# Optimization experiments

Measured on AMD Instinct MI355X. Metric: run time of the kernel, lower is better.

## Reference

```python
import jax, jax.numpy as jnp
import numpy as np

N, E, R, L = 20000, 160000, 3, 2
IN, HID, H, OUT = 64, 128, 16, 1
FH = HID // H   # per-head dim = 8
HD2 = HID // 2  # MLP bottleneck = 64


def setup_inputs() -> dict:
    key = jax.random.key(0)
    ks = iter(jax.random.split(key, 40))
    def w(*shape):
        return jax.random.normal(next(ks), shape, jnp.float32) * 0.05
    inp = dict(
        inputs=jax.random.normal(next(ks), (N, IN), jnp.float32),
        src=jax.random.randint(next(ks), (R, E), 0, N, dtype=jnp.int32),
        dst=jax.random.randint(next(ks), (R, E), 0, N, dtype=jnp.int32),
        e1_W=w(IN, HID), e1_b=jnp.zeros(HID), e_g=jnp.ones(HID), e_bt=jnp.zeros(HID),
        e2_W=w(HID, HID), e2_b=jnp.zeros(HID),
        gat_W=w(L, R, HID, HID), gat_al=w(L, R, H, FH), gat_ar=w(L, R, H, FH),
        gat_b=jnp.zeros((L, R, HID)),
        attn_p=w(L, R, HID),
        m1_W=w(L, HID, HD2), m1_b=jnp.zeros((L, HD2)), m_g=jnp.ones((L, HD2)), m_bt=jnp.zeros((L, HD2)),
        m2_W=w(L, HD2, HID), m2_b=jnp.zeros((L, HID)),
        d1_W=w(HID, HD2), d1_b=jnp.zeros(HD2), d_g=jnp.ones(HD2), d_bt=jnp.zeros(HD2),
        d2_W=w(HD2, OUT), d2_b=jnp.zeros(OUT),
    )
    return inp


def _bn(x, g, b):
    # BatchNorm1d, training mode: biased batch statistics, eps=1e-5
    mu = x.mean(0)
    var = jnp.mean((x - mu) ** 2, 0)
    return g * (x - mu) * jax.lax.rsqrt(var + 1e-5) + b


def _mlp(x, W1, b1, g, bt, W2, b2, skip=False):
    h = jax.nn.relu(_bn(x @ W1 + b1, g, bt))
    o = h @ W2 + b2
    return o + h if skip else o


def _gat(x, W, al, ar, b, src, dst):
    # single-relation DGL GATConv (feat_drop=attn_drop=0, neg_slope=0.2, bias)
    z = (x @ W).reshape(N, H, FH)                 # [N,H,FH]
    el = (z * al).sum(-1)                          # [N,H]
    er = (z * ar).sum(-1)                          # [N,H]
    e = jax.nn.leaky_relu(el[src] + er[dst], 0.2)  # [E,H]
    m = jax.ops.segment_max(e, dst, num_segments=N)
    m = jnp.where(jnp.isfinite(m), m, 0.0)
    ex = jnp.exp(e - m[dst])
    s = jax.ops.segment_sum(ex, dst, num_segments=N)
    alpha = ex / s[dst]                            # edge softmax over in-edges
    out = jax.ops.segment_sum(alpha[:, :, None] * z[src], dst, num_segments=N)
    return out.reshape(N, HID) + b                 # flatten heads + bias


def reference(inputs, src, dst, e1_W, e1_b, e_g, e_bt, e2_W, e2_b,
              gat_W, gat_al, gat_ar, gat_b, attn_p,
              m1_W, m1_b, m_g, m_bt, m2_W, m2_b,
              d1_W, d1_b, d_g, d_bt, d2_W, d2_b):
    h = _mlp(inputs, e1_W, e1_b, e_g, e_bt, e2_W, e2_b, skip=True)  # embed, skip
    gat_v = jax.vmap(_gat, in_axes=(None, 0, 0, 0, 0, 0, 0))        # over relations
    for l in range(L):
        stacked = gat_v(h, gat_W[l], gat_al[l], gat_ar[l], gat_b[l], src, dst)  # [R,N,HID]
        w = jax.nn.softmax(attn_p[l], axis=0)        # per-dim softmax over relations [R,HID]
        v = jnp.einsum('rnf,rf->nf', stacked, w)     # attn-weighted relation agg
        h = _mlp(v, m1_W[l], m1_b[l], m_g[l], m_bt[l], m2_W[l], m2_b[l]) + h
    return _mlp(h, d1_W, d1_b, d_g, d_bt, d2_W, d2_b)
```

## Files before the change

### kernel.cpp

```cpp
#include <hip/hip_runtime.h>
#include <math.h>

constexpr int kN   = 20000;
constexpr int kE   = 160000;
constexpr int kR   = 3;
constexpr int kL   = 2;
constexpr int kIN  = 64;
constexpr int kHID = 128;
constexpr int kH   = 16;
constexpr int kFH  = 8;
constexpr int kHD2 = 64;

typedef __bf16 bf16x8 __attribute__((ext_vector_type(8)));
typedef float  f32x4  __attribute__((ext_vector_type(4)));

__device__ __forceinline__ bf16x8 ldfrag(const __bf16* p) {
  return __builtin_bit_cast(bf16x8, *(const uint4*)p);
}
__device__ __forceinline__ f32x4 MF(bf16x8 a, bf16x8 b, f32x4 c) {
  return __builtin_amdgcn_mfma_f32_16x16x32_bf16(a, b, c, 0, 0, 0);
}

__device__ __forceinline__ void splitrow(const float* __restrict__ rowbase, int koff,
                                         bool bn, const float* scS, const float* shS,
                                         bf16x8& hi, bf16x8& lo) {
  float4 xa = *(const float4*)(rowbase + koff);
  float4 xb = *(const float4*)(rowbase + koff + 4);
  float x[8] = {xa.x, xa.y, xa.z, xa.w, xb.x, xb.y, xb.z, xb.w};
  union { __bf16 b[8]; bf16x8 v; } uh, ul;
#pragma unroll
  for (int e = 0; e < 8; e++) {
    float y = x[e];
    if (bn) y = fmaxf(fmaf(y, scS[koff + e], shS[koff + e]), 0.f);
    __bf16 hb = (__bf16)y;
    uh.b[e] = hb;
    ul.b[e] = (__bf16)(y - (float)hb);
  }
  hi = uh.v; lo = ul.v;
}

__global__ __launch_bounds__(256) void mgemm_kernel(
    const float* __restrict__ A, const __bf16* __restrict__ WT,
    const float* __restrict__ bias, const float* __restrict__ resf, int resmode,
    const float* __restrict__ bnstat, const float* __restrict__ bng,
    const float* __restrict__ bnbt, float invn,
    float* __restrict__ statS,
    float* __restrict__ Cf, __bf16* __restrict__ Chi,
    const float* __restrict__ alb, const float* __restrict__ arb,
    float* __restrict__ elb, float* __restrict__ erb,
    int n, int k, int m, long wstride, long cstride) {
  __shared__ __bf16 Bh[64][136];
  __shared__ __bf16 Bl[64][136];
  __shared__ float scS[128], shS[128];
  const int t  = threadIdx.x;
  const int w  = t >> 6;
  const int l  = t & 63;
  const int lr = l & 15;
  const int lg = l >> 4;
  const int rb = blockIdx.x * 128 + w * 32;
  const int c0 = blockIdx.y * 64;
  const __bf16* Whi = WT + (size_t)blockIdx.z * wstride;
  const __bf16* Wlo = Whi + (size_t)k * m;
  if (Chi) Chi += (size_t)blockIdx.z * cstride;
  const float* al = alb ? alb + blockIdx.z * kHID : nullptr;
  const float* ar = arb ? arb + blockIdx.z * kHID : nullptr;
  if (elb) { elb += blockIdx.z * 16; erb += blockIdx.z * 16; }

  const bool bn = bnstat != nullptr;
  if (bn && t < k) {
    float mu  = bnstat[t] * invn;
    float var = bnstat[k + t] * invn - mu * mu;
    float s = bng[t] * rsqrtf(var + 1e-5f);
    scS[t] = s; shS[t] = bnbt[t] - mu * s;
  }
  const int kseg = k >> 3;
  for (int idx = t; idx < 64 * kseg; idx += 256) {
    int col = idx / kseg, seg = idx - col * kseg;
    *(uint4*)&Bh[col][seg * 8] = *(const uint4*)&Whi[(size_t)(c0 + col) * k + seg * 8];
    *(uint4*)&Bl[col][seg * 8] = *(const uint4*)&Wlo[(size_t)(c0 + col) * k + seg * 8];
  }
  __syncthreads();

  int r0 = rb + lr;      if (r0 > n - 1) r0 = n - 1;
  int r1 = rb + 16 + lr; if (r1 > n - 1) r1 = n - 1;
  f32x4 acc[2][4] = {};

  for (int ks = 0; ks < (k >> 5); ks++) {
    const int koff = ks * 32 + lg * 8;
    bf16x8 a0h, a0l, a1h, a1l;
    splitrow(&A[(size_t)r0 * k], koff, bn, scS, shS, a0h, a0l);
    splitrow(&A[(size_t)r1 * k], koff, bn, scS, shS, a1h, a1l);
#pragma unroll
    for (int j = 0; j < 4; j++) {
      bf16x8 bh = ldfrag(&Bh[j * 16 + lr][koff]);
      bf16x8 bl = ldfrag(&Bl[j * 16 + lr][koff]);
      acc[0][j] = MF(a0h, bh, acc[0][j]);
      acc[0][j] = MF(a0l, bh, acc[0][j]);
      acc[0][j] = MF(a0h, bl, acc[0][j]);
      acc[1][j] = MF(a1h, bh, acc[1][j]);
      acc[1][j] = MF(a1l, bh, acc[1][j]);
      acc[1][j] = MF(a1h, bl, acc[1][j]);
    }
  }

  float s[4] = {}, s2[4] = {};
#pragma unroll
  for (int i = 0; i < 2; i++) {
#pragma unroll
    for (int q = 0; q < 4; q++) {
      int row = rb + i * 16 + lg * 4 + q;
      bool ok = row < n;
#pragma unroll
      for (int j = 0; j < 4; j++) {
        int col = c0 + j * 16 + lr;
        float v = acc[i][j][q];
        if (bias) v += bias[col];
        size_t off = (size_t)row * m + col;
        if (ok) {
          if (resmode == 1) v += resf[off];
          else if (resmode == 2) v += fmaxf(fmaf(resf[off], scS[col], shS[col]), 0.f);
          if (Cf) Cf[off] = v;
          if (Chi) Chi[off] = (__bf16)v;
          s[j] += v; s2[j] += v * v;
        }
      }
    }
  }
  if (statS) {
    __syncthreads();
    float* red = (float*)&Bh[0][0];
#pragma unroll
    for (int j = 0; j < 4; j++) {
      float a = s[j], b = s2[j];
      a += __shfl_xor(a, 16, 64); a += __shfl_xor(a, 32, 64);
      b += __shfl_xor(b, 16, 64); b += __shfl_xor(b, 32, 64);
      if (lg == 0) { red[w * 64 + j * 16 + lr] = a; red[256 + w * 64 + j * 16 + lr] = b; }
    }
    __syncthreads();
    if (t < 64) {
      float a = red[t] + red[64 + t] + red[128 + t] + red[192 + t];
      float b = red[256 + t] + red[320 + t] + red[384 + t] + red[448 + t];
      atomicAdd(&statS[c0 + t], a);
      atomicAdd(&statS[m + c0 + t], b);
    }
  }
  if (al) {
#pragma unroll
    for (int i = 0; i < 2; i++) {
#pragma unroll
      for (int q = 0; q < 4; q++) {
        int row = rb + i * 16 + lg * 4 + q;
#pragma unroll
        for (int j = 0; j < 4; j++) {
          int col = c0 + j * 16 + lr;
          float zv = acc[i][j][q];
          float pl = zv * al[col];
          float pr = zv * ar[col];
          pl += __shfl_xor(pl, 1, 64); pl += __shfl_xor(pl, 2, 64); pl += __shfl_xor(pl, 4, 64);
          pr += __shfl_xor(pr, 1, 64); pr += __shfl_xor(pr, 2, 64); pr += __shfl_xor(pr, 4, 64);
          if ((lr & 7) == 0 && row < n) {
            int hd = col >> 3;
            elb[(size_t)row * 48 + hd] = pl;
            erb[(size_t)row * 48 + hd] = pr;
          }
        }
      }
    }
  }
}

struct WDesc { const float* src; long doff; int k, m; };
struct WDescs { WDesc d[13]; };
__global__ void wprep_kernel(WDescs ds, __bf16* __restrict__ wt) {
  WDesc dd = ds.d[blockIdx.y];
  int idx = blockIdx.x * 256 + threadIdx.x;
  if (idx >= dd.k * dd.m) return;
  int row = idx / dd.m, col = idx - row * dd.m;
  float v = dd.src[idx];
  __bf16 hb = (__bf16)v;
  __bf16 lb = (__bf16)(v - (float)hb);
  wt[dd.doff + (size_t)col * dd.k + row] = hb;
  wt[dd.doff + (size_t)dd.k * dd.m + (size_t)col * dd.k + row] = lb;
}

__global__ void hist_kernel(const int* __restrict__ dst, int* __restrict__ deg) {
  int r = blockIdx.y;
  int e = blockIdx.x * 256 + threadIdx.x;
  if (e < kE) atomicAdd(&deg[r * kN + dst[r * kE + e]], 1);
}

__global__ __launch_bounds__(1024) void csr_scan_kernel(const int* __restrict__ deg,
                                                        int* __restrict__ rowptr) {
  const int r = blockIdx.y;
  const int* dg = deg + r * kN;
  int* rp = rowptr + r * (kN + 1);
  const int t = threadIdx.x;
  constexpr int C = (kN + 1023) / 1024;
  const int base = t * C;
  int sum = 0;
#pragma unroll
  for (int i = 0; i < C; i++) {
    int j = base + i;
    if (j < kN) sum += dg[j];
  }
  __shared__ int warpTot[16];
  int lane = t & 63, wid = t >> 6;
  int v = sum;
  for (int off = 1; off < 64; off <<= 1) {
    int y = __shfl_up(v, off, 64);
    if (lane >= off) v += y;
  }
  if (lane == 63) warpTot[wid] = v;
  __syncthreads();
  int wadd = 0;
#pragma unroll
  for (int i = 0; i < 16; i++) if (i < wid) wadd += warpTot[i];
  int run = wadd + v - sum;
#pragma unroll
  for (int i = 0; i < C; i++) {
    int j = base + i;
    if (j < kN) { rp[j] = run; run += dg[j]; }
  }
  if (t == 1023) rp[kN] = run;
}

__global__ void scatter_kernel(const int* __restrict__ src, const int* __restrict__ dst,
                               const int* __restrict__ rowptr, int* __restrict__ cursor,
                               int* __restrict__ col) {
  int r = blockIdx.y;
  int e = blockIdx.x * 256 + threadIdx.x;
  if (e < kE) {
    int d = dst[r * kE + e];
    int p = atomicAdd(&cursor[r * kN + d], 1);
    col[r * kE + rowptr[r * (kN + 1) + d] + p] = src[r * kE + e];
  }
}

__global__ void gat3_kernel(const int* __restrict__ rowptr, const int* __restrict__ colidx,
                            const ushort* __restrict__ z, const float* __restrict__ elb,
                            const float* __restrict__ erb,
                            const float* __restrict__ attn_pl, const float* __restrict__ gat_bl,
                            float* __restrict__ vv) {
  __shared__ float wsmS[kR * kHID], cvecS[kHID];
  int t = threadIdx.x;
  if (t < kHID) {
    float p0 = attn_pl[t], p1 = attn_pl[kHID + t], p2 = attn_pl[2 * kHID + t];
    float mx = fmaxf(p0, fmaxf(p1, p2));
    float e0 = __expf(p0 - mx), e1 = __expf(p1 - mx), e2 = __expf(p2 - mx);
    float si = 1.f / (e0 + e1 + e2);
    wsmS[t] = e0 * si; wsmS[kHID + t] = e1 * si; wsmS[2 * kHID + t] = e2 * si;
    cvecS[t] = (e0 * gat_bl[t] + e1 * gat_bl[kHID + t] + e2 * gat_bl[2 * kHID + t]) * si;
  }
  __syncthreads();
  int idx = blockIdx.x * 256 + t;
  if (idx >= kN * kH) return;
  int d = idx >> 4, hh = idx & 15;
  const int fo = hh << 3;
  float out[kFH];
#pragma unroll
  for (int f = 0; f < kFH; f++) out[f] = cvecS[fo + f];
  for (int r = 0; r < kR; r++) {
    const int* rp = rowptr + r * (kN + 1);
    const int* ci = colidx + (size_t)r * kE;
    const ushort* zr = z + (size_t)r * kN * kHID;
    const int ro = r * 16;
    float erd = erb[(size_t)d * 48 + ro + hh];
    int beg = rp[d], end = rp[d + 1];
    float s = 0.f;
    float acc[kFH] = {};
    int p = beg;
    for (; p + 4 <= end; p += 4) {
      int svA = ci[p], svB = ci[p + 1], svC = ci[p + 2], svD = ci[p + 3];
      float vA = elb[(size_t)svA * 48 + ro + hh];
      float vB = elb[(size_t)svB * 48 + ro + hh];
      float vC = elb[(size_t)svC * 48 + ro + hh];
      float vD = elb[(size_t)svD * 48 + ro + hh];
      uint4 zA = *(const uint4*)(zr + ((size_t)svA << 7) + fo);
      uint4 zB = *(const uint4*)(zr + ((size_t)svB << 7) + fo);
      uint4 zC = *(const uint4*)(zr + ((size_t)svC << 7) + fo);
      uint4 zD = *(const uint4*)(zr + ((size_t)svD << 7) + fo);
      uint4 zz[4] = {zA, zB, zC, zD};
      float vv4[4] = {vA, vB, vC, vD};
#pragma unroll
      for (int u = 0; u < 4; u++) {
        float v = vv4[u] + erd;
        v = v > 0.f ? v : 0.2f * v;
        float ex = __expf(v);
        s += ex;
        acc[0] = fmaf(ex, __uint_as_float(zz[u].x << 16),         acc[0]);
        acc[1] = fmaf(ex, __uint_as_float(zz[u].x & 0xffff0000u), acc[1]);
        acc[2] = fmaf(ex, __uint_as_float(zz[u].y << 16),         acc[2]);
        acc[3] = fmaf(ex, __uint_as_float(zz[u].y & 0xffff0000u), acc[3]);
        acc[4] = fmaf(ex, __uint_as_float(zz[u].z << 16),         acc[4]);
        acc[5] = fmaf(ex, __uint_as_float(zz[u].z & 0xffff0000u), acc[5]);
        acc[6] = fmaf(ex, __uint_as_float(zz[u].w << 16),         acc[6]);
        acc[7] = fmaf(ex, __uint_as_float(zz[u].w & 0xffff0000u), acc[7]);
      }
    }
    for (; p < end; p++) {
      int sv = ci[p];
      float v = elb[(size_t)sv * 48 + ro + hh] + erd;
      v = v > 0.f ? v : 0.2f * v;
      float ex = __expf(v);
      s += ex;
      uint4 zz = *(const uint4*)(zr + ((size_t)sv << 7) + fo);
      acc[0] = fmaf(ex, __uint_as_float(zz.x << 16),         acc[0]);
      acc[1] = fmaf(ex, __uint_as_float(zz.x & 0xffff0000u), acc[1]);
      acc[2] = fmaf(ex, __uint_as_float(zz.y << 16),         acc[2]);
      acc[3] = fmaf(ex, __uint_as_float(zz.y & 0xffff0000u), acc[3]);
      acc[4] = fmaf(ex, __uint_as_float(zz.z << 16),         acc[4]);
      acc[5] = fmaf(ex, __uint_as_float(zz.z & 0xffff0000u), acc[5]);
      acc[6] = fmaf(ex, __uint_as_float(zz.w << 16),         acc[6]);
      acc[7] = fmaf(ex, __uint_as_float(zz.w & 0xffff0000u), acc[7]);
    }
    float inv = s > 0.f ? 1.f / s : 0.f;
    const float* wp = wsmS + r * kHID + fo;
#pragma unroll
    for (int f = 0; f < kFH; f++) out[f] = fmaf(wp[f] * inv, acc[f], out[f]);
  }
  float4* vp = (float4*)(vv + ((size_t)d << 7) + fo);
  vp[0] = make_float4(out[0], out[1], out[2], out[3]);
  vp[1] = make_float4(out[4], out[5], out[6], out[7]);
}

__global__ void gemv_out_kernel(const float* __restrict__ A, const float* __restrict__ statS,
                                const float* __restrict__ g, const float* __restrict__ bt,
                                float invn, const float* __restrict__ w,
                                const float* __restrict__ b, float* __restrict__ out,
                                int n, int k) {
  __shared__ float scS[kHD2], shS[kHD2];
  int t = threadIdx.x;
  if (t < k) {
    float mu  = statS[t] * invn;
    float var = statS[k + t] * invn - mu * mu;
    float s = g[t] * rsqrtf(var + 1e-5f);
    scS[t] = s; shS[t] = bt[t] - mu * s;
  }
  __syncthreads();
  int i = blockIdx.x * 256 + t;
  if (i >= n) return;
  const float4* a = (const float4*)(A + (size_t)i * k);
  float acc = b[0];
  for (int j4 = 0; j4 < k / 4; j4++) {
    float4 x = a[j4];
    int c = j4 * 4;
    acc = fmaf(fmaxf(fmaf(x.x, scS[c],     shS[c]),     0.f), w[c],     acc);
    acc = fmaf(fmaxf(fmaf(x.y, scS[c + 1], shS[c + 1]), 0.f), w[c + 1], acc);
    acc = fmaf(fmaxf(fmaf(x.z, scS[c + 2], shS[c + 2]), 0.f), w[c + 2], acc);
    acc = fmaf(fmaxf(fmaf(x.w, scS[c + 3], shS[c + 3]), 0.f), w[c + 3], acc);
  }
  out[i] = acc;
}

extern "C" void kernel_launch(void* const* d_in, const int* in_sizes, int n_in,
                              void* d_out, int out_size, void* d_ws, size_t ws_size,
                              hipStream_t stream) {
  const float* inputs = (const float*)d_in[0];
  const int*   src    = (const int*)d_in[1];
  const int*   dst    = (const int*)d_in[2];
  const float* e1_W   = (const float*)d_in[3];
  const float* e1_b   = (const float*)d_in[4];
  const float* e_g    = (const float*)d_in[5];
  const float* e_bt   = (const float*)d_in[6];
  const float* e2_W   = (const float*)d_in[7];
  const float* e2_b   = (const float*)d_in[8];
  const float* gat_W  = (const float*)d_in[9];
  const float* gat_al = (const float*)d_in[10];
  const float* gat_ar = (const float*)d_in[11];
  const float* gat_b  = (const float*)d_in[12];
  const float* attn_p = (const float*)d_in[13];
  const float* m1_W   = (const float*)d_in[14];
  const float* m1_b   = (const float*)d_in[15];
  const float* m_g    = (const float*)d_in[16];
  const float* m_bt   = (const float*)d_in[17];
  const float* m2_W   = (const float*)d_in[18];
  const float* m2_b   = (const float*)d_in[19];
  const float* d1_W   = (const float*)d_in[20];
  const float* d1_b   = (const float*)d_in[21];
  const float* d_g    = (const float*)d_in[22];
  const float* d_bt   = (const float*)d_in[23];
  const float* d2_W   = (const float*)d_in[24];
  const float* d2_b   = (const float*)d_in[25];

  float* ws = (float*)d_ws;
  size_t o = 0;
  float*  h     = ws + o; o += (size_t)kN * kHID;
  float*  bufA  = ws + o; o += (size_t)kN * kHID;
  float*  vv    = ws + o; o += (size_t)kN * kHID;
  float*  elbuf = ws + o; o += (size_t)kN * 48;
  float*  erbuf = ws + o; o += (size_t)kN * 48;
  __bf16* z     = (__bf16*)(ws + o); o += (size_t)kR * kN * kHID / 2;
  __bf16* wt    = (__bf16*)(ws + o); o += 327680 / 2;
  int* degcur   = (int*)(ws + o); o += (size_t)6 * kN;
  float* stats  = ws + o; o += 640;
  int* rowptr   = (int*)(ws + o); o += (size_t)kR * (kN + 1);
  int* colidx   = (int*)(ws + o); o += (size_t)kR * kE;
  (void)ws_size; (void)in_sizes; (void)n_in; (void)out_size;

  int* deg    = degcur;
  int* cursor = degcur + 3 * kN;
  float* stat_e1 = stats;
  float* stat_m1[2] = {stats + 256, stats + 384};
  float* stat_d1 = stats + 512;

  const long kWE1 = 0, kWE2 = 16384, kWZ = 49152;
  const long kWM1_0 = 245760, kWM1_1 = 262144, kWM2_0 = 278528, kWM2_1 = 294912, kWD1 = 311296;

  auto nb = [](long t) { return (int)((t + 255) / 256); };
  const dim3 gE(nb(kE), kR);
  const dim3 gM128((kN + 127) / 128, 2, 1);
  const dim3 gM64((kN + 127) / 128, 1, 1);
  const dim3 gMZ((kN + 127) / 128, 2, kR);
  const float invn = 1.0f / kN;
  float* F0 = nullptr; const float* cF0 = nullptr;

  hipMemsetAsync(degcur, 0, ((size_t)6 * kN + 640) * sizeof(int), stream);
  hist_kernel<<<gE, 256, 0, stream>>>(dst, deg);
  csr_scan_kernel<<<dim3(1, kR), 1024, 0, stream>>>(deg, rowptr);
  scatter_kernel<<<gE, 256, 0, stream>>>(src, dst, rowptr, cursor, colidx);

  WDescs wd;
  wd.d[0] = {e1_W, kWE1, kIN, kHID};
  wd.d[1] = {e2_W, kWE2, kHID, kHID};
  for (int i = 0; i < 6; i++) wd.d[2 + i] = {gat_W + (size_t)i * 16384, kWZ + (long)i * 32768, kHID, kHID};
  wd.d[8]  = {m1_W,        kWM1_0, kHID, kHD2};
  wd.d[9]  = {m1_W + 8192, kWM1_1, kHID, kHD2};
  wd.d[10] = {m2_W,        kWM2_0, kHD2, kHID};
  wd.d[11] = {m2_W + 8192, kWM2_1, kHD2, kHID};
  wd.d[12] = {d1_W,        kWD1,   kHID, kHD2};
  wprep_kernel<<<dim3(64, 13), 256, 0, stream>>>(wd, wt);

  mgemm_kernel<<<gM128, 256, 0, stream>>>(inputs, wt + kWE1, e1_b, cF0, 0,
                                          cF0, cF0, cF0, invn, stat_e1, bufA, nullptr,
                                          cF0, cF0, F0, F0, kN, kIN, kHID, 0, 0);
  mgemm_kernel<<<gM128, 256, 0, stream>>>(bufA, wt + kWE2, e2_b, bufA, 2,
                                          stat_e1, e_g, e_bt, invn, F0, h, nullptr,
                                          cF0, cF0, F0, F0, kN, kHID, kHID, 0, 0);

  for (int l = 0; l < kL; l++) {
    mgemm_kernel<<<gMZ, 256, 0, stream>>>(h, wt + kWZ + (long)l * 3 * 32768, cF0, cF0, 0,
                                          cF0, cF0, cF0, invn, F0, F0, z,
                                          gat_al + (size_t)l * kR * kHID,
                                          gat_ar + (size_t)l * kR * kHID, elbuf, erbuf,
                                          kN, kHID, kHID, 32768, (long)kN * kHID);
    gat3_kernel<<<nb((long)kN * kH), 256, 0, stream>>>(rowptr, colidx, (const ushort*)z,
                                             elbuf, erbuf,
                                             attn_p + (size_t)l * kR * kHID,
                                             gat_b + (size_t)l * kR * kHID, vv);
    mgemm_kernel<<<gM64, 256, 0, stream>>>(vv, wt + (l ? kWM1_1 : kWM1_0),
                                           m1_b + (size_t)l * kHD2, cF0, 0,
                                           cF0, cF0, cF0, invn, stat_m1[l], bufA, nullptr,
                                           cF0, cF0, F0, F0, kN, kHID, kHD2, 0, 0);
    mgemm_kernel<<<gM128, 256, 0, stream>>>(bufA, wt + (l ? kWM2_1 : kWM2_0),
                                            m2_b + (size_t)l * kHID, h, 1,
                                            stat_m1[l], m_g + (size_t)l * kHD2,
                                            m_bt + (size_t)l * kHD2, invn, F0, h, nullptr,
                                            cF0, cF0, F0, F0, kN, kHD2, kHID, 0, 0);
  }

  mgemm_kernel<<<gM64, 256, 0, stream>>>(h, wt + kWD1, d1_b, cF0, 0,
                                         cF0, cF0, cF0, invn, stat_d1, bufA, nullptr,
                                         cF0, cF0, F0, F0, kN, kHID, kHD2, 0, 0);
  gemv_out_kernel<<<nb(kN), 256, 0, stream>>>(bufA, stat_d1, d_g, d_bt, invn,
                                              d2_W, d2_b, (float*)d_out, kN, kHD2);
}
```

Before: 342.8 us.

## Store GAT features and attention logits head-major to localize gathers

The z projection, el/er logits and the GAT output are now stored head-major ([head][node][8]) instead of node-major. The GAT kernel runs one head per grid row, so each thread gathers from a compact per-head array. This is meant to improve cache reuse and locality of the random neighbour gathers. The downstream GEMM gains a strided A-load mode to read the head-major output, and the z GEMM writes transposed with scattered 2-byte stores, which may cost some store efficiency.

```diff
diff --git a/kernel.cpp b/kernel.cpp
--- a/kernel.cpp
+++ b/kernel.cpp
@@ -21,11 +21,11 @@
   return __builtin_amdgcn_mfma_f32_16x16x32_bf16(a, b, c, 0, 0, 0);
 }
 
-__device__ __forceinline__ void splitrow(const float* __restrict__ rowbase, int koff,
+__device__ __forceinline__ void splitrow(const float* __restrict__ p, int koff,
                                          bool bn, const float* scS, const float* shS,
                                          bf16x8& hi, bf16x8& lo) {
-  float4 xa = *(const float4*)(rowbase + koff);
-  float4 xb = *(const float4*)(rowbase + koff + 4);
+  float4 xa = *(const float4*)p;
+  float4 xb = *(const float4*)(p + 4);
   float x[8] = {xa.x, xa.y, xa.z, xa.w, xb.x, xb.y, xb.z, xb.w};
   union { __bf16 b[8]; bf16x8 v; } uh, ul;
 #pragma unroll
@@ -48,7 +48,7 @@
     float* __restrict__ Cf, __bf16* __restrict__ Chi,
     const float* __restrict__ alb, const float* __restrict__ arb,
     float* __restrict__ elb, float* __restrict__ erb,
-    int n, int k, int m, long wstride, long cstride) {
+    int n, int k, int m, long wstride, long cstride, int amode, int cmode) {
   __shared__ __bf16 Bh[64][136];
   __shared__ __bf16 Bl[64][136];
   __shared__ float scS[128], shS[128];
@@ -64,7 +64,7 @@
   if (Chi) Chi += (size_t)blockIdx.z * cstride;
   const float* al = alb ? alb + blockIdx.z * kHID : nullptr;
   const float* ar = arb ? arb + blockIdx.z * kHID : nullptr;
-  if (elb) { elb += blockIdx.z * 16; erb += blockIdx.z * 16; }
+  if (elb) { elb += (size_t)blockIdx.z * 16 * n; erb += (size_t)blockIdx.z * 16 * n; }
 
   const bool bn = bnstat != nullptr;
   if (bn && t < k) {
@@ -87,9 +87,13 @@
 
   for (int ks = 0; ks < (k >> 5); ks++) {
     const int koff = ks * 32 + lg * 8;
+    const float* p0 = amode ? (A + (size_t)koff * n + (size_t)r0 * 8)
+                            : (A + (size_t)r0 * k + koff);
+    const float* p1 = amode ? (A + (size_t)koff * n + (size_t)r1 * 8)
+                            : (A + (size_t)r1 * k + koff);
     bf16x8 a0h, a0l, a1h, a1l;
-    splitrow(&A[(size_t)r0 * k], koff, bn, scS, shS, a0h, a0l);
-    splitrow(&A[(size_t)r1 * k], koff, bn, scS, shS, a1h, a1l);
+    splitrow(p0, koff, bn, scS, shS, a0h, a0l);
+    splitrow(p1, koff, bn, scS, shS, a1h, a1l);
 #pragma unroll
     for (int j = 0; j < 4; j++) {
       bf16x8 bh = ldfrag(&Bh[j * 16 + lr][koff]);
@@ -120,7 +124,10 @@
           if (resmode == 1) v += resf[off];
           else if (resmode == 2) v += fmaxf(fmaf(resf[off], scS[col], shS[col]), 0.f);
           if (Cf) Cf[off] = v;
-          if (Chi) Chi[off] = (__bf16)v;
+          if (Chi) {
+            if (cmode) Chi[((size_t)(col >> 3) * n + row) * 8 + (col & 7)] = (__bf16)v;
+            else Chi[off] = (__bf16)v;
+          }
           s[j] += v; s2[j] += v * v;
         }
       }
@@ -160,8 +167,8 @@
           pr += __shfl_xor(pr, 1, 64); pr += __shfl_xor(pr, 2, 64); pr += __shfl_xor(pr, 4, 64);
           if ((lr & 7) == 0 && row < n) {
             int hd = col >> 3;
-            elb[(size_t)row * 48 + hd] = pl;
-            erb[(size_t)row * 48 + hd] = pr;
+            elb[(size_t)hd * n + row] = pl;
+            erb[(size_t)hd * n + row] = pr;
           }
         }
       }
@@ -237,10 +244,10 @@
 }
 
 __global__ void gat3_kernel(const int* __restrict__ rowptr, const int* __restrict__ colidx,
-                            const ushort* __restrict__ z, const float* __restrict__ elb,
-                            const float* __restrict__ erb,
+                            const ushort* __restrict__ z, const float* __restrict__ elh,
+                            const float* __restrict__ erh,
                             const float* __restrict__ attn_pl, const float* __restrict__ gat_bl,
-                            float* __restrict__ vv) {
+                            float* __restrict__ vvh) {
   __shared__ float wsmS[kR * kHID], cvecS[kHID];
   int t = threadIdx.x;
   if (t < kHID) {
@@ -252,9 +259,9 @@
     cvecS[t] = (e0 * gat_bl[t] + e1 * gat_bl[kHID + t] + e2 * gat_bl[2 * kHID + t]) * si;
   }
   __syncthreads();
-  int idx = blockIdx.x * 256 + t;
-  if (idx >= kN * kH) return;
-  int d = idx >> 4, hh = idx & 15;
+  int d = blockIdx.x * 256 + t;
+  if (d >= kN) return;
+  const int hh = blockIdx.y;
   const int fo = hh << 3;
   float out[kFH];
 #pragma unroll
@@ -262,23 +269,20 @@
   for (int r = 0; r < kR; r++) {
     const int* rp = rowptr + r * (kN + 1);
     const int* ci = colidx + (size_t)r * kE;
-    const ushort* zr = z + (size_t)r * kN * kHID;
-    const int ro = r * 16;
-    float erd = erb[(size_t)d * 48 + ro + hh];
+    const ushort* zr = z + (size_t)(r * kH + hh) * kN * 8;
+    const float* elp = elh + (size_t)(r * kH + hh) * kN;
+    float erd = erh[(size_t)(r * kH + hh) * kN + d];
     int beg = rp[d], end = rp[d + 1];
     float s = 0.f;
     float acc[kFH] = {};
     int p = beg;
     for (; p + 4 <= end; p += 4) {
       int svA = ci[p], svB = ci[p + 1], svC = ci[p + 2], svD = ci[p + 3];
-      float vA = elb[(size_t)svA * 48 + ro + hh];
-      float vB = elb[(size_t)svB * 48 + ro + hh];
-      float vC = elb[(size_t)svC * 48 + ro + hh];
-      float vD = elb[(size_t)svD * 48 + ro + hh];
-      uint4 zA = *(const uint4*)(zr + ((size_t)svA << 7) + fo);
-      uint4 zB = *(const uint4*)(zr + ((size_t)svB << 7) + fo);
-      uint4 zC = *(const uint4*)(zr + ((size_t)svC << 7) + fo);
-      uint4 zD = *(const uint4*)(zr + ((size_t)svD << 7) + fo);
+      float vA = elp[svA], vB = elp[svB], vC = elp[svC], vD = elp[svD];
+      uint4 zA = *(const uint4*)(zr + (size_t)svA * 8);
+      uint4 zB = *(const uint4*)(zr + (size_t)svB * 8);
+      uint4 zC = *(const uint4*)(zr + (size_t)svC * 8);
+      uint4 zD = *(const uint4*)(zr + (size_t)svD * 8);
       uint4 zz[4] = {zA, zB, zC, zD};
       float vv4[4] = {vA, vB, vC, vD};
 #pragma unroll
@@ -299,11 +303,11 @@
     }
     for (; p < end; p++) {
       int sv = ci[p];
-      float v = elb[(size_t)sv * 48 + ro + hh] + erd;
+      float v = elp[sv] + erd;
       v = v > 0.f ? v : 0.2f * v;
       float ex = __expf(v);
       s += ex;
-      uint4 zz = *(const uint4*)(zr + ((size_t)sv << 7) + fo);
+      uint4 zz = *(const uint4*)(zr + (size_t)sv * 8);
       acc[0] = fmaf(ex, __uint_as_float(zz.x << 16),         acc[0]);
       acc[1] = fmaf(ex, __uint_as_float(zz.x & 0xffff0000u), acc[1]);
       acc[2] = fmaf(ex, __uint_as_float(zz.y << 16),         acc[2]);
@@ -318,7 +322,7 @@
 #pragma unroll
     for (int f = 0; f < kFH; f++) out[f] = fmaf(wp[f] * inv, acc[f], out[f]);
   }
-  float4* vp = (float4*)(vv + ((size_t)d << 7) + fo);
+  float4* vp = (float4*)(vvh + ((size_t)hh * kN + d) * 8);
   vp[0] = make_float4(out[0], out[1], out[2], out[3]);
   vp[1] = make_float4(out[4], out[5], out[6], out[7]);
 }
@@ -386,9 +390,9 @@
   size_t o = 0;
   float*  h     = ws + o; o += (size_t)kN * kHID;
   float*  bufA  = ws + o; o += (size_t)kN * kHID;
-  float*  vv    = ws + o; o += (size_t)kN * kHID;
-  float*  elbuf = ws + o; o += (size_t)kN * 48;
-  float*  erbuf = ws + o; o += (size_t)kN * 48;
+  float*  vvh   = ws + o; o += (size_t)kN * kHID;
+  float*  elh   = ws + o; o += (size_t)kR * kH * kN;
+  float*  erh   = ws + o; o += (size_t)kR * kH * kN;
   __bf16* z     = (__bf16*)(ws + o); o += (size_t)kR * kN * kHID / 2;
   __bf16* wt    = (__bf16*)(ws + o); o += 327680 / 2;
   int* degcur   = (int*)(ws + o); o += (size_t)6 * kN;
@@ -411,6 +415,7 @@
   const dim3 gM128((kN + 127) / 128, 2, 1);
   const dim3 gM64((kN + 127) / 128, 1, 1);
   const dim3 gMZ((kN + 127) / 128, 2, kR);
+  const dim3 gG3(nb(kN), kH);
   const float invn = 1.0f / kN;
   float* F0 = nullptr; const float* cF0 = nullptr;
 
@@ -432,35 +437,34 @@
 
   mgemm_kernel<<<gM128, 256, 0, stream>>>(inputs, wt + kWE1, e1_b, cF0, 0,
                                           cF0, cF0, cF0, invn, stat_e1, bufA, nullptr,
-                                          cF0, cF0, F0, F0, kN, kIN, kHID, 0, 0);
+                                          cF0, cF0, F0, F0, kN, kIN, kHID, 0, 0, 0, 0);
   mgemm_kernel<<<gM128, 256, 0, stream>>>(bufA, wt + kWE2, e2_b, bufA, 2,
                                           stat_e1, e_g, e_bt, invn, F0, h, nullptr,
-                                          cF0, cF0, F0, F0, kN, kHID, kHID, 0, 0);
+                                          cF0, cF0, F0, F0, kN, kHID, kHID, 0, 0, 0, 0);
 
   for (int l = 0; l < kL; l++) {
     mgemm_kernel<<<gMZ, 256, 0, stream>>>(h, wt + kWZ + (long)l * 3 * 32768, cF0, cF0, 0,
                                           cF0, cF0, cF0, invn, F0, F0, z,
                                           gat_al + (size_t)l * kR * kHID,
-                                          gat_ar + (size_t)l * kR * kHID, elbuf, erbuf,
-                                          kN, kHID, kHID, 32768, (long)kN * kHID);
-    gat3_kernel<<<nb((long)kN * kH), 256, 0, stream>>>(rowptr, colidx, (const ushort*)z,
-                                             elbuf, erbuf,
-                                             attn_p + (size_t)l * kR * kHID,
-                                             gat_b + (size_t)l * kR * kHID, vv);
-    mgemm_kernel<<<gM64, 256, 0, stream>>>(vv, wt + (l ? kWM1_1 : kWM1_0),
+                                          gat_ar + (size_t)l * kR * kHID, elh, erh,
+                                          kN, kHID, kHID, 32768, (long)kN * kHID, 0, 1);
+    gat3_kernel<<<gG3, 256, 0, stream>>>(rowptr, colidx, (const ushort*)z, elh, erh,
+                                         attn_p + (size_t)l * kR * kHID,
+                                         gat_b + (size_t)l * kR * kHID, vvh);
+    mgemm_kernel<<<gM64, 256, 0, stream>>>(vvh, wt + (l ? kWM1_1 : kWM1_0),
                                            m1_b + (size_t)l * kHD2, cF0, 0,
                                            cF0, cF0, cF0, invn, stat_m1[l], bufA, nullptr,
-                                           cF0, cF0, F0, F0, kN, kHID, kHD2, 0, 0);
+                                           cF0, cF0, F0, F0, kN, kHID, kHD2, 0, 0, 1, 0);
     mgemm_kernel<<<gM128, 256, 0, stream>>>(bufA, wt + (l ? kWM2_1 : kWM2_0),
                                             m2_b + (size_t)l * kHID, h, 1,
                                             stat_m1[l], m_g + (size_t)l * kHD2,
                                             m_bt + (size_t)l * kHD2, invn, F0, h, nullptr,
-                                            cF0, cF0, F0, F0, kN, kHD2, kHID, 0, 0);
+                                            cF0, cF0, F0, F0, kN, kHD2, kHID, 0, 0, 0, 0);
   }
 
   mgemm_kernel<<<gM64, 256, 0, stream>>>(h, wt + kWD1, d1_b, cF0, 0,
                                          cF0, cF0, cF0, invn, stat_d1, bufA, nullptr,
-                                         cF0, cF0, F0, F0, kN, kHID, kHD2, 0, 0);
+                                         cF0, cF0, F0, F0, kN, kHID, kHD2, 0, 0, 0, 0);
   gemv_out_kernel<<<nb(kN), 256, 0, stream>>>(bufA, stat_d1, d_g, d_bt, invn,
                                               d2_W, d2_b, (float*)d_out, kN, kHD2);
 }
```

Measured after the change: 463.0 us. 1.35x slower.
